# Kernel tuning notes

Measured on AMD Instinct MI355X. Metric: run time of the kernel, lower is better.

The kernel has to match this reference:

```python
import jax, jax.numpy as jnp
import numpy as np

B, E, N, F, D = 4, 8192, 1024, 512, 512
ALPHA = 0.2
NEG = -1e9  # keras Softmax large-negative masking constant


def setup_inputs() -> dict:
    key = jax.random.key(0)
    k_nodes, k_src, k_dst, k_w, k_a = jax.random.split(key, 5)
    nodes = jax.random.normal(k_nodes, (B, N, F), dtype=jnp.float32)
    src = jax.random.randint(k_src, (B, E), 0, N)
    dst = jax.random.randint(k_dst, (B, E), 0, N)
    Cmat = jax.nn.one_hot(src, N, dtype=jnp.float32)  # [B,E,N] source incidence
    Nmat = jax.nn.one_hot(dst, N, dtype=jnp.float32)  # [B,E,N] target incidence
    mask = jnp.ones((B, N, N), dtype=bool)  # present in input tuple but unused by call()
    w = jax.random.normal(k_w, (F, D), dtype=jnp.float32) * 0.05
    attention = jax.random.normal(k_a, (2 * D, 1), dtype=jnp.float32) * 0.05
    return {"nodes": nodes, "Cmat": Cmat, "Nmat": Nmat, "mask": mask,
            "w": w, "attention": attention}


def reference(nodes, Cmat, Nmat, mask, w, attention):
    z = jnp.matmul(nodes, w)                       # [B,N,D]
    z1 = jnp.matmul(Cmat, z)                       # [B,E,D] source embeddings
    z2 = jnp.matmul(Nmat, z)                       # [B,E,D] target embeddings
    couple = jnp.concatenate([z1, z2], axis=-1)    # [B,E,2D]
    att = jax.nn.leaky_relu(jnp.matmul(couple, attention), ALPHA)  # [B,E,1]
    att_t = jnp.swapaxes(att, -1, -2)              # [B,1,E]
    Cmat_t = jnp.swapaxes(Cmat, -1, -2)            # [B,N,E]
    scores = jnp.matmul(Cmat_t * att_t, Nmat)      # [B,N,N] per-edge score scattered
    adj = jnp.matmul(Cmat_t, Nmat)                 # [B,N,N] adjacency
    # keras Softmax(mask=adj): logits += (1 - cast(adj)) * NEG, softmax over last axis
    logits = scores + (1.0 - adj) * (-NEG) * -1.0 if False else scores + (1.0 - adj) * NEG
    adj_norm = jax.nn.softmax(logits, axis=-1) * adj
    out = jax.nn.leaky_relu(jnp.matmul(adj_norm, z), ALPHA)  # [B,N,D]
    return out
```

## Files before the change

### kernel.cpp

```cpp
#include <hip/hip_runtime.h>
#include <hip/hip_bf16.h>
#include <math.h>

#define BB 4
#define EE 8192
#define NN 1024
#define FF 512
#define DD 512
#define ALPHA 0.2f
#define SLOTS 64

typedef __attribute__((ext_vector_type(8))) short short8;
typedef __attribute__((ext_vector_type(4))) float f32x4;

static __device__ __forceinline__ float leaky(float x) { return x > 0.f ? x : ALPHA * x; }

static __device__ __forceinline__ float wave_sum(float v) {
#pragma unroll
    for (int m = 32; m >= 1; m >>= 1) v += __shfl_xor(v, m);
    return v;
}
static __device__ __forceinline__ float wave_max(float v) {
#pragma unroll
    for (int m = 32; m >= 1; m >>= 1) v = fmaxf(v, __shfl_xor(v, m));
    return v;
}
static __device__ __forceinline__ float dot4(float4 a, float4 b) {
    return a.x * b.x + a.y * b.y + a.z * b.z + a.w * b.w;
}
static __device__ __forceinline__ short8 cvt8(float4 a, float4 b) {
    __hip_bfloat16 t[8];
    t[0] = __float2bfloat16(a.x); t[1] = __float2bfloat16(a.y);
    t[2] = __float2bfloat16(a.z); t[3] = __float2bfloat16(a.w);
    t[4] = __float2bfloat16(b.x); t[5] = __float2bfloat16(b.y);
    t[6] = __float2bfloat16(b.z); t[7] = __float2bfloat16(b.w);
    return *(short8*)t;
}
static __device__ __forceinline__ float b2f(short s) {
    unsigned u = ((unsigned)(unsigned short)s) << 16;
    float f;
    __builtin_memcpy(&f, &u, 4);
    return f;
}
static __device__ __forceinline__ short f2b(float f) {
    __hip_bfloat16 h = __float2bfloat16(f);
    short s;
    __builtin_memcpy(&s, &h, 2);
    return s;
}
static __device__ __forceinline__ int find2(uint4 a, uint4 b, int lane) {
    unsigned za = a.x | a.y | a.z | a.w, zb = b.x | b.y | b.z | b.w;
    unsigned long long m = __ballot((za | zb) != 0u);
    if (!m) return -1;
    int il = za ? (lane * 4 + (a.x ? 0 : (a.y ? 1 : (a.z ? 2 : 3))))
                : (256 + lane * 4 + (b.x ? 0 : (b.y ? 1 : (b.z ? 2 : 3))));
    return __shfl(il, (int)__ffsll(m) - 1);
}
static __device__ __forceinline__ int find1(uint4 v, int lane) {
    unsigned nz = v.x | v.y | v.z | v.w;
    unsigned long long m = __ballot(nz != 0u);
    if (!m) return -1;
    int il = lane * 4 + (v.x ? 0 : (v.y ? 1 : (v.z ? 2 : 3)));
    return __shfl(il, (int)__ffsll(m) - 1);
}

__global__ __launch_bounds__(256) void k_prep(const float* __restrict__ w,
                                              const float* __restrict__ attn,
                                              __hip_bfloat16* __restrict__ BT,
                                              float* __restrict__ wa1, float* __restrict__ wa2,
                                              int* __restrict__ cur) {
    int bx = blockIdx.x;
    if (bx < 64) {
        __shared__ float tile[64][65];
        int tk = bx >> 3, tn = bx & 7;
        int k0 = tk * 64, n0 = tn * 64;
#pragma unroll
        for (int it = 0; it < 16; ++it) {
            int id = it * 256 + threadIdx.x;
            int r = id >> 6, c = id & 63;
            tile[r][c] = w[(size_t)(k0 + r) * DD + n0 + c];
        }
        __syncthreads();
#pragma unroll
        for (int it = 0; it < 16; ++it) {
            int id = it * 256 + threadIdx.x;
            int r = id >> 6, c = id & 63;
            BT[(size_t)(n0 + r) * FF + k0 + c] = __float2bfloat16(tile[c][r]);
        }
        return;
    }
    if (bx < 192) {
        int f = (bx - 64) * 4 + (threadIdx.x >> 6);
        int lane = threadIdx.x & 63;
        const float4* wr = (const float4*)(w + (size_t)f * DD);
        const float4* a1p = (const float4*)attn;
        const float4* a2p = (const float4*)(attn + DD);
        float4 wv0 = wr[lane], wv1 = wr[64 + lane];
        float s1 = dot4(wv0, a1p[lane]) + dot4(wv1, a1p[64 + lane]);
        float s2 = dot4(wv0, a2p[lane]) + dot4(wv1, a2p[64 + lane]);
        s1 = wave_sum(s1);
        s2 = wave_sum(s2);
        if (lane == 0) {
            wa1[f] = s1;
            wa2[f] = s2;
        }
        return;
    }
    int4* cp = (int4*)cur;
    int4 z4 = {0, 0, 0, 0};
#pragma unroll
    for (int j = 0; j < 4; j++) cp[threadIdx.x * 4 + j] = z4;
}

#define BM 128
#define BN 64
#define BK 32
#define NEX 8192
__global__ __launch_bounds__(256) void k_mega(const float* __restrict__ nodes,
                                              const __hip_bfloat16* __restrict__ BTbf,
                                              const float* __restrict__ wa1,
                                              const float* __restrict__ wa2,
                                              const float* __restrict__ C,
                                              const float* __restrict__ Nm,
                                              short* __restrict__ Z16,
                                              float* __restrict__ p1, float* __restrict__ p2,
                                              int* __restrict__ cur, int* __restrict__ sDst) {
    __shared__ short As[BM][BK + 8];
    __shared__ short Bs[BN][BK + 8];
    int bx = blockIdx.x;
    int t = threadIdx.x;
    int lane = t & 63;
    if (bx < 256) {
        int m0 = (bx & 31) * BM;
        int n0 = (bx >> 5) * BN;
        int wid = t >> 6;
        int wm = wid & 1, wn = wid >> 1;
        f32x4 acc[4][2] = {};
        const short* Bg = (const short*)BTbf;
        for (int k0 = 0; k0 < FF; k0 += BK) {
#pragma unroll
            for (int s = 0; s < 2; s++) {
                int cid = t + s * 256;
                int r = cid >> 2, cc = cid & 3;
                const float4* ap = (const float4*)&nodes[(size_t)(m0 + r) * FF + k0 + cc * 8];
                *(short8*)&As[r][cc * 8] = cvt8(ap[0], ap[1]);
            }
            {
                int r = t >> 2, cc = t & 3;
                *(short8*)&Bs[r][cc * 8] = *(const short8*)&Bg[(size_t)(n0 + r) * FF + k0 + cc * 8];
            }
            __syncthreads();
            short8 af[4];
            short8 bf[2];
#pragma unroll
            for (int m = 0; m < 4; m++)
                af[m] = *(const short8*)&As[wm * 64 + m * 16 + (lane & 15)][(lane >> 4) * 8];
#pragma unroll
            for (int n = 0; n < 2; n++)
                bf[n] = *(const short8*)&Bs[wn * 32 + n * 16 + (lane & 15)][(lane >> 4) * 8];
#pragma unroll
            for (int m = 0; m < 4; m++)
#pragma unroll
                for (int n = 0; n < 2; n++)
                    acc[m][n] = __builtin_amdgcn_mfma_f32_16x16x32_bf16(af[m], bf[n], acc[m][n], 0, 0, 0);
            __syncthreads();
        }
#pragma unroll
        for (int m = 0; m < 4; m++)
#pragma unroll
            for (int n = 0; n < 2; n++)
#pragma unroll
                for (int r = 0; r < 4; r++) {
                    int row = m0 + wm * 64 + m * 16 + (lane >> 4) * 4 + r;
                    int col = n0 + wn * 32 + n * 16 + (lane & 15);
                    Z16[(size_t)row * DD + col] = f2b(acc[m][n][r]);
                }
        return;
    }
    if (bx < 256 + NEX) {
        int widx = (bx - 256) * 4 + (t >> 6);
        const uint4* rc = (const uint4*)(C + (size_t)widx * NN);
        const uint4* rn = (const uint4*)(Nm + (size_t)widx * NN);
        uint4 a0 = rc[lane], a1 = rc[64 + lane];
        uint4 b0 = rn[lane], b1 = rn[64 + lane];
        int s = find2(a0, a1, lane);
        int d = find2(b0, b1, lane);
#pragma unroll 1
        for (int c = 2; c < 4 && (s < 0 || d < 0); ++c) {
            uint4 va, vb;
            bool needS = s < 0, needD = d < 0;
            if (needS) va = rc[c * 64 + lane];
            if (needD) vb = rn[c * 64 + lane];
            if (needS) {
                int r = find1(va, lane);
                if (r >= 0) s = c * 256 + r;
            }
            if (needD) {
                int r = find1(vb, lane);
                if (r >= 0) d = c * 256 + r;
            }
        }
        if (lane == 0) {
            int b = widx >> 13;
            int row = b * NN + s;
            int pos = atomicAdd(&cur[row], 1);
            if (pos < SLOTS) sDst[row * SLOTS + pos] = d;
        }
        return;
    }
    int rid = (bx - 256 - NEX) * 4 + (t >> 6);
    const float4* nr = (const float4*)(nodes + (size_t)rid * FF);
    const float4* w1p = (const float4*)wa1;
    const float4* w2p = (const float4*)wa2;
    float4 v0 = nr[lane], v1 = nr[64 + lane];
    float s1 = dot4(v0, w1p[lane]) + dot4(v1, w1p[64 + lane]);
    float s2 = dot4(v0, w2p[lane]) + dot4(v1, w2p[64 + lane]);
    s1 = wave_sum(s1);
    s2 = wave_sum(s2);
    if (lane == 0) {
        p1[rid] = s1;
        p2[rid] = s2;
    }
}

__global__ __launch_bounds__(256) void k_out(const int* __restrict__ cur,
                                             const int* __restrict__ sDst,
                                             const float* __restrict__ p1,
                                             const float* __restrict__ p2,
                                             const short* __restrict__ Z16,
                                             float* __restrict__ out) {
    int rid = (blockIdx.x * 256 + threadIdx.x) >> 6;
    int lane = threadIdx.x & 63;
    if (rid >= BB * NN) return;
    int K = cur[rid];
    K = K > SLOTS ? SLOTS : K;
    int base = rid * SLOTS;
    int b = rid >> 10;
    float* op = out + (size_t)rid * DD + lane * 8;
    if (K == 0) {
        float4 z4 = {0.f, 0.f, 0.f, 0.f};
        *(float4*)op = z4;
        *(float4*)(op + 4) = z4;
        return;
    }
    float p1row = p1[rid];
    int de = (lane < K) ? sDst[base + lane] : -1;
    float ae = (lane < K) ? leaky(p1row + p2[(b << 10) + de]) : 0.f;
    float S = 0.f;
    int c = 0, firstk = 64;
    for (int k = 0; k < K; k++) {
        int dk = __shfl(de, k);
        float ak = __shfl(ae, k);
        bool mt = (lane < K) && (dk == de);
        if (mt) {
            S += ak;
            c++;
            if (k < firstk) firstk = k;
        }
    }
    float logit = (lane < K) ? (S + (float)(c - 1) * 1e9f) : -INFINITY;
    float M = wave_max(logit);
    float contrib = (lane < K && firstk == lane) ? __expf(logit - M) : 0.f;
    float Dsum = wave_sum(contrib);
    float wgt = (lane < K) ? __expf(logit - M) / Dsum : 0.f;
    const short* Zb = Z16 + ((size_t)(b << 10)) * DD;
    float acc[8] = {0.f, 0.f, 0.f, 0.f, 0.f, 0.f, 0.f, 0.f};
#pragma unroll
    for (int k = 0; k < 32; k++) {
        if (k >= K) break;
        int dj = __shfl(de, k);
        float wk = __shfl(wgt, k);
        short8 zv = *(const short8*)(Zb + (size_t)dj * DD + lane * 8);
#pragma unroll
        for (int j = 0; j < 8; j++) acc[j] += wk * b2f(zv[j]);
    }
    for (int k = 32; k < K; k++) {
        int dj = __shfl(de, k);
        float wk = __shfl(wgt, k);
        short8 zv = *(const short8*)(Zb + (size_t)dj * DD + lane * 8);
#pragma unroll
        for (int j = 0; j < 8; j++) acc[j] += wk * b2f(zv[j]);
    }
    float4 o0, o1;
    o0.x = leaky(acc[0]); o0.y = leaky(acc[1]); o0.z = leaky(acc[2]); o0.w = leaky(acc[3]);
    o1.x = leaky(acc[4]); o1.y = leaky(acc[5]); o1.z = leaky(acc[6]); o1.w = leaky(acc[7]);
    *(float4*)op = o0;
    *(float4*)(op + 4) = o1;
}

extern "C" void kernel_launch(void* const* d_in, const int* in_sizes, int n_in,
                              void* d_out, int out_size, void* d_ws, size_t ws_size,
                              hipStream_t stream) {
    const float* nodes = (const float*)d_in[0];
    const float* Cmat = (const float*)d_in[1];
    const float* Nmat = (const float*)d_in[2];
    const float* w = (const float*)d_in[4];
    const float* attn = (const float*)d_in[5];
    float* out = (float*)d_out;

    char* ws = (char*)d_ws;
    size_t off = 0;
    auto alloc = [&](size_t bytes) -> void* {
        void* p = ws + off;
        off += (bytes + 255) & ~(size_t)255;
        return p;
    };
    short* Z16 = (short*)alloc((size_t)BB * NN * DD * 2);
    __hip_bfloat16* BT = (__hip_bfloat16*)alloc((size_t)FF * DD * 2);
    float* wa1 = (float*)alloc((size_t)FF * 4);
    float* wa2 = (float*)alloc((size_t)FF * 4);
    int* cur = (int*)alloc((size_t)BB * NN * 4);
    int* sDst = (int*)alloc((size_t)BB * NN * SLOTS * 4);
    float* p1 = (float*)alloc((size_t)BB * NN * 4);
    float* p2 = (float*)alloc((size_t)BB * NN * 4);

    k_prep<<<193, 256, 0, stream>>>(w, attn, BT, wa1, wa2, cur);
    k_mega<<<256 + NEX + 1024, 256, 0, stream>>>(nodes, BT, wa1, wa2, Cmat, Nmat,
                                                 Z16, p1, p2, cur, sDst);
    k_out<<<1024, 256, 0, stream>>>(cur, sDst, p1, p2, Z16, out);
}
```

Measured before the change: 51.58 us.

## Compute attention projections from bf16 Z in output kernel instead of precomputed p1/p2

Drops the w·attention precompute and the per-node p1/p2 dot-product blocks from the prep and mega kernels. The output kernel now computes both attention projections directly from the bf16 Z rows it already gathers, using a wave reduction per neighbour. The edge-scan loop is also simplified to a single loop starting at chunk 0. This cuts blocks and launches in the earlier stages but adds per-neighbour Z loads and reductions in k_out, and the projections now use bf16-rounded Z rather than fp32 nodes.

New measurement: 57.67 us. 11.8% more time.

```diff
diff --git a/kernel.cpp b/kernel.cpp
--- a/kernel.cpp
+++ b/kernel.cpp
@@ -9,6 +9,8 @@
 #define DD 512
 #define ALPHA 0.2f
 #define SLOTS 64
+#define NGEMM 256
+#define NEX 8192
 
 typedef __attribute__((ext_vector_type(8))) short short8;
 typedef __attribute__((ext_vector_type(4))) float f32x4;
@@ -24,9 +26,6 @@
 #pragma unroll
     for (int m = 32; m >= 1; m >>= 1) v = fmaxf(v, __shfl_xor(v, m));
     return v;
-}
-static __device__ __forceinline__ float dot4(float4 a, float4 b) {
-    return a.x * b.x + a.y * b.y + a.z * b.z + a.w * b.w;
 }
 static __device__ __forceinline__ short8 cvt8(float4 a, float4 b) {
     __hip_bfloat16 t[8];
@@ -48,13 +47,9 @@
     __builtin_memcpy(&s, &h, 2);
     return s;
 }
-static __device__ __forceinline__ int find2(uint4 a, uint4 b, int lane) {
-    unsigned za = a.x | a.y | a.z | a.w, zb = b.x | b.y | b.z | b.w;
-    unsigned long long m = __ballot((za | zb) != 0u);
-    if (!m) return -1;
-    int il = za ? (lane * 4 + (a.x ? 0 : (a.y ? 1 : (a.z ? 2 : 3))))
-                : (256 + lane * 4 + (b.x ? 0 : (b.y ? 1 : (b.z ? 2 : 3))));
-    return __shfl(il, (int)__ffsll(m) - 1);
+static __device__ __forceinline__ float dot8(short8 z, float4 alo, float4 ahi) {
+    return b2f(z[0]) * alo.x + b2f(z[1]) * alo.y + b2f(z[2]) * alo.z + b2f(z[3]) * alo.w +
+           b2f(z[4]) * ahi.x + b2f(z[5]) * ahi.y + b2f(z[6]) * ahi.z + b2f(z[7]) * ahi.w;
 }
 static __device__ __forceinline__ int find1(uint4 v, int lane) {
     unsigned nz = v.x | v.y | v.z | v.w;
@@ -65,9 +60,7 @@
 }
 
 __global__ __launch_bounds__(256) void k_prep(const float* __restrict__ w,
-                                              const float* __restrict__ attn,
                                               __hip_bfloat16* __restrict__ BT,
-                                              float* __restrict__ wa1, float* __restrict__ wa2,
                                               int* __restrict__ cur) {
     int bx = blockIdx.x;
     if (bx < 64) {
@@ -89,23 +82,6 @@
         }
         return;
     }
-    if (bx < 192) {
-        int f = (bx - 64) * 4 + (threadIdx.x >> 6);
-        int lane = threadIdx.x & 63;
-        const float4* wr = (const float4*)(w + (size_t)f * DD);
-        const float4* a1p = (const float4*)attn;
-        const float4* a2p = (const float4*)(attn + DD);
-        float4 wv0 = wr[lane], wv1 = wr[64 + lane];
-        float s1 = dot4(wv0, a1p[lane]) + dot4(wv1, a1p[64 + lane]);
-        float s2 = dot4(wv0, a2p[lane]) + dot4(wv1, a2p[64 + lane]);
-        s1 = wave_sum(s1);
-        s2 = wave_sum(s2);
-        if (lane == 0) {
-            wa1[f] = s1;
-            wa2[f] = s2;
-        }
-        return;
-    }
     int4* cp = (int4*)cur;
     int4 z4 = {0, 0, 0, 0};
 #pragma unroll
@@ -115,22 +91,18 @@
 #define BM 128
 #define BN 64
 #define BK 32
-#define NEX 8192
 __global__ __launch_bounds__(256) void k_mega(const float* __restrict__ nodes,
                                               const __hip_bfloat16* __restrict__ BTbf,
-                                              const float* __restrict__ wa1,
-                                              const float* __restrict__ wa2,
                                               const float* __restrict__ C,
                                               const float* __restrict__ Nm,
                                               short* __restrict__ Z16,
-                                              float* __restrict__ p1, float* __restrict__ p2,
                                               int* __restrict__ cur, int* __restrict__ sDst) {
     __shared__ short As[BM][BK + 8];
     __shared__ short Bs[BN][BK + 8];
     int bx = blockIdx.x;
     int t = threadIdx.x;
     int lane = t & 63;
-    if (bx < 256) {
+    if (bx < NGEMM) {
         int m0 = (bx & 31) * BM;
         int n0 = (bx >> 5) * BN;
         int wid = t >> 6;
@@ -177,56 +149,36 @@
                 }
         return;
     }
-    if (bx < 256 + NEX) {
-        int widx = (bx - 256) * 4 + (t >> 6);
-        const uint4* rc = (const uint4*)(C + (size_t)widx * NN);
-        const uint4* rn = (const uint4*)(Nm + (size_t)widx * NN);
-        uint4 a0 = rc[lane], a1 = rc[64 + lane];
-        uint4 b0 = rn[lane], b1 = rn[64 + lane];
-        int s = find2(a0, a1, lane);
-        int d = find2(b0, b1, lane);
+    int widx = (bx - NGEMM) * 4 + (t >> 6);
+    const uint4* rc = (const uint4*)(C + (size_t)widx * NN);
+    const uint4* rn = (const uint4*)(Nm + (size_t)widx * NN);
+    int s = -1, d = -1;
 #pragma unroll 1
-        for (int c = 2; c < 4 && (s < 0 || d < 0); ++c) {
-            uint4 va, vb;
-            bool needS = s < 0, needD = d < 0;
-            if (needS) va = rc[c * 64 + lane];
-            if (needD) vb = rn[c * 64 + lane];
-            if (needS) {
-                int r = find1(va, lane);
-                if (r >= 0) s = c * 256 + r;
-            }
-            if (needD) {
-                int r = find1(vb, lane);
-                if (r >= 0) d = c * 256 + r;
-            }
-        }
-        if (lane == 0) {
-            int b = widx >> 13;
-            int row = b * NN + s;
-            int pos = atomicAdd(&cur[row], 1);
-            if (pos < SLOTS) sDst[row * SLOTS + pos] = d;
-        }
-        return;
-    }
-    int rid = (bx - 256 - NEX) * 4 + (t >> 6);
-    const float4* nr = (const float4*)(nodes + (size_t)rid * FF);
-    const float4* w1p = (const float4*)wa1;
-    const float4* w2p = (const float4*)wa2;
-    float4 v0 = nr[lane], v1 = nr[64 + lane];
-    float s1 = dot4(v0, w1p[lane]) + dot4(v1, w1p[64 + lane]);
-    float s2 = dot4(v0, w2p[lane]) + dot4(v1, w2p[64 + lane]);
-    s1 = wave_sum(s1);
-    s2 = wave_sum(s2);
+    for (int c = 0; c < 4 && ((s < 0) | (d < 0)); ++c) {
+        uint4 va, vb;
+        bool ns = s < 0, nd = d < 0;
+        if (ns) va = rc[c * 64 + lane];
+        if (nd) vb = rn[c * 64 + lane];
+        if (ns) {
+            int r = find1(va, lane);
+            if (r >= 0) s = c * 256 + r;
+        }
+        if (nd) {
+            int r = find1(vb, lane);
+            if (r >= 0) d = c * 256 + r;
+        }
+    }
     if (lane == 0) {
-        p1[rid] = s1;
-        p2[rid] = s2;
+        int b = widx >> 13;
+        int row = b * NN + s;
+        int pos = atomicAdd(&cur[row], 1);
+        if (pos < SLOTS) sDst[row * SLOTS + pos] = d;
     }
 }
 
 __global__ __launch_bounds__(256) void k_out(const int* __restrict__ cur,
                                              const int* __restrict__ sDst,
-                                             const float* __restrict__ p1,
-                                             const float* __restrict__ p2,
+                                             const float* __restrict__ attn,
                                              const short* __restrict__ Z16,
                                              float* __restrict__ out) {
     int rid = (blockIdx.x * 256 + threadIdx.x) >> 6;
@@ -243,9 +195,21 @@
         *(float4*)(op + 4) = z4;
         return;
     }
-    float p1row = p1[rid];
+    const float4* at4 = (const float4*)attn;
+    float4 a1lo = at4[lane * 2], a1hi = at4[lane * 2 + 1];
+    float4 a2lo = at4[128 + lane * 2], a2hi = at4[128 + lane * 2 + 1];
+    const short* Zb = Z16 + ((size_t)(b << 10)) * DD;
+    short8 zr = *(const short8*)(Z16 + (size_t)rid * DD + lane * 8);
+    float p1row = wave_sum(dot8(zr, a1lo, a1hi));
     int de = (lane < K) ? sDst[base + lane] : -1;
-    float ae = (lane < K) ? leaky(p1row + p2[(b << 10) + de]) : 0.f;
+    float p2mine = 0.f;
+    for (int k = 0; k < K; k++) {
+        int dk = __shfl(de, k);
+        short8 zv = *(const short8*)(Zb + (size_t)dk * DD + lane * 8);
+        float sum = wave_sum(dot8(zv, a2lo, a2hi));
+        if (lane == k) p2mine = sum;
+    }
+    float ae = (lane < K) ? leaky(p1row + p2mine) : 0.f;
     float S = 0.f;
     int c = 0, firstk = 64;
     for (int k = 0; k < K; k++) {
@@ -263,7 +227,6 @@
     float contrib = (lane < K && firstk == lane) ? __expf(logit - M) : 0.f;
     float Dsum = wave_sum(contrib);
     float wgt = (lane < K) ? __expf(logit - M) / Dsum : 0.f;
-    const short* Zb = Z16 + ((size_t)(b << 10)) * DD;
     float acc[8] = {0.f, 0.f, 0.f, 0.f, 0.f, 0.f, 0.f, 0.f};
 #pragma unroll
     for (int k = 0; k < 32; k++) {
@@ -307,15 +270,10 @@
     };
     short* Z16 = (short*)alloc((size_t)BB * NN * DD * 2);
     __hip_bfloat16* BT = (__hip_bfloat16*)alloc((size_t)FF * DD * 2);
-    float* wa1 = (float*)alloc((size_t)FF * 4);
-    float* wa2 = (float*)alloc((size_t)FF * 4);
     int* cur = (int*)alloc((size_t)BB * NN * 4);
     int* sDst = (int*)alloc((size_t)BB * NN * SLOTS * 4);
-    float* p1 = (float*)alloc((size_t)BB * NN * 4);
-    float* p2 = (float*)alloc((size_t)BB * NN * 4);
-
-    k_prep<<<193, 256, 0, stream>>>(w, attn, BT, wa1, wa2, cur);
-    k_mega<<<256 + NEX + 1024, 256, 0, stream>>>(nodes, BT, wa1, wa2, Cmat, Nmat,
-                                                 Z16, p1, p2, cur, sDst);
-    k_out<<<1024, 256, 0, stream>>>(cur, sDst, p1, p2, Z16, out);
-}
+
+    k_prep<<<65, 256, 0, stream>>>(w, BT, cur);
+    k_mega<<<NGEMM + NEX, 256, 0, stream>>>(nodes, BT, Cmat, Nmat, Z16, cur, sDst);
+    k_out<<<1024, 256, 0, stream>>>(cur, sDst, attn, Z16, out);
+}
```

## Drop prep kernel: load w directly in GEMM and fuse attention projections into epilogue

Applied to the files above, without the earlier changes.

Removes the separate prep kernel that transposed w to bf16 and computed w·attention. The GEMM now reads fp32 w with strided column loads, converting to bf16 on the fly, and computes p1/p2 in its epilogue from the accumulators via shuffle reductions and atomicAdd. cur, p1 and p2 are zeroed with one memset, which relies on them being contiguous in the workspace. The change saves one launch and the extra per-row dot-product blocks, at the cost of uncoalesced, redundant B loads, float atomics (nondeterministic summation order) and p1/p2 now computed from Z in fp32 accumulators rather than from fp32 nodes.

Measured after the change: 52.42 us. About the same (+1.6%).

```diff
diff --git a/kernel.cpp b/kernel.cpp
--- a/kernel.cpp
+++ b/kernel.cpp
@@ -9,6 +9,8 @@
 #define DD 512
 #define ALPHA 0.2f
 #define SLOTS 64
+#define NGEMM 256
+#define NEX 8192
 
 typedef __attribute__((ext_vector_type(8))) short short8;
 typedef __attribute__((ext_vector_type(4))) float f32x4;
@@ -24,9 +26,6 @@
 #pragma unroll
     for (int m = 32; m >= 1; m >>= 1) v = fmaxf(v, __shfl_xor(v, m));
     return v;
-}
-static __device__ __forceinline__ float dot4(float4 a, float4 b) {
-    return a.x * b.x + a.y * b.y + a.z * b.z + a.w * b.w;
 }
 static __device__ __forceinline__ short8 cvt8(float4 a, float4 b) {
     __hip_bfloat16 t[8];
@@ -64,62 +63,12 @@
     return __shfl(il, (int)__ffsll(m) - 1);
 }
 
-__global__ __launch_bounds__(256) void k_prep(const float* __restrict__ w,
-                                              const float* __restrict__ attn,
-                                              __hip_bfloat16* __restrict__ BT,
-                                              float* __restrict__ wa1, float* __restrict__ wa2,
-                                              int* __restrict__ cur) {
-    int bx = blockIdx.x;
-    if (bx < 64) {
-        __shared__ float tile[64][65];
-        int tk = bx >> 3, tn = bx & 7;
-        int k0 = tk * 64, n0 = tn * 64;
-#pragma unroll
-        for (int it = 0; it < 16; ++it) {
-            int id = it * 256 + threadIdx.x;
-            int r = id >> 6, c = id & 63;
-            tile[r][c] = w[(size_t)(k0 + r) * DD + n0 + c];
-        }
-        __syncthreads();
-#pragma unroll
-        for (int it = 0; it < 16; ++it) {
-            int id = it * 256 + threadIdx.x;
-            int r = id >> 6, c = id & 63;
-            BT[(size_t)(n0 + r) * FF + k0 + c] = __float2bfloat16(tile[c][r]);
-        }
-        return;
-    }
-    if (bx < 192) {
-        int f = (bx - 64) * 4 + (threadIdx.x >> 6);
-        int lane = threadIdx.x & 63;
-        const float4* wr = (const float4*)(w + (size_t)f * DD);
-        const float4* a1p = (const float4*)attn;
-        const float4* a2p = (const float4*)(attn + DD);
-        float4 wv0 = wr[lane], wv1 = wr[64 + lane];
-        float s1 = dot4(wv0, a1p[lane]) + dot4(wv1, a1p[64 + lane]);
-        float s2 = dot4(wv0, a2p[lane]) + dot4(wv1, a2p[64 + lane]);
-        s1 = wave_sum(s1);
-        s2 = wave_sum(s2);
-        if (lane == 0) {
-            wa1[f] = s1;
-            wa2[f] = s2;
-        }
-        return;
-    }
-    int4* cp = (int4*)cur;
-    int4 z4 = {0, 0, 0, 0};
-#pragma unroll
-    for (int j = 0; j < 4; j++) cp[threadIdx.x * 4 + j] = z4;
-}
-
 #define BM 128
 #define BN 64
 #define BK 32
-#define NEX 8192
 __global__ __launch_bounds__(256) void k_mega(const float* __restrict__ nodes,
-                                              const __hip_bfloat16* __restrict__ BTbf,
-                                              const float* __restrict__ wa1,
-                                              const float* __restrict__ wa2,
+                                              const float* __restrict__ w,
+                                              const float* __restrict__ attn,
                                               const float* __restrict__ C,
                                               const float* __restrict__ Nm,
                                               short* __restrict__ Z16,
@@ -130,13 +79,13 @@
     int bx = blockIdx.x;
     int t = threadIdx.x;
     int lane = t & 63;
-    if (bx < 256) {
+    if (bx < NGEMM) {
         int m0 = (bx & 31) * BM;
         int n0 = (bx >> 5) * BN;
         int wid = t >> 6;
         int wm = wid & 1, wn = wid >> 1;
+        int bc = t & 63, bkr = t >> 6;
         f32x4 acc[4][2] = {};
-        const short* Bg = (const short*)BTbf;
         for (int k0 = 0; k0 < FF; k0 += BK) {
 #pragma unroll
             for (int s = 0; s < 2; s++) {
@@ -146,8 +95,11 @@
                 *(short8*)&As[r][cc * 8] = cvt8(ap[0], ap[1]);
             }
             {
-                int r = t >> 2, cc = t & 3;
-                *(short8*)&Bs[r][cc * 8] = *(const short8*)&Bg[(size_t)(n0 + r) * FF + k0 + cc * 8];
+                short tmpb[8];
+#pragma unroll
+                for (int i = 0; i < 8; i++)
+                    tmpb[i] = f2b(w[(size_t)(k0 + bkr * 8 + i) * DD + n0 + bc]);
+                *(short8*)&Bs[bc][bkr * 8] = *(short8*)tmpb;
             }
             __syncthreads();
             short8 af[4];
@@ -165,8 +117,15 @@
                     acc[m][n] = __builtin_amdgcn_mfma_f32_16x16x32_bf16(af[m], bf[n], acc[m][n], 0, 0, 0);
             __syncthreads();
         }
-#pragma unroll
-        for (int m = 0; m < 4; m++)
+        float a1c[2], a2c[2];
+#pragma unroll
+        for (int n = 0; n < 2; n++) {
+            int col = n0 + wn * 32 + n * 16 + (lane & 15);
+            a1c[n] = attn[col];
+            a2c[n] = attn[DD + col];
+        }
+#pragma unroll
+        for (int m = 0; m < 4; m++) {
 #pragma unroll
             for (int n = 0; n < 2; n++)
 #pragma unroll
@@ -175,51 +134,51 @@
                     int col = n0 + wn * 32 + n * 16 + (lane & 15);
                     Z16[(size_t)row * DD + col] = f2b(acc[m][n][r]);
                 }
+#pragma unroll
+            for (int r = 0; r < 4; r++) {
+                float v1 = acc[m][0][r] * a1c[0] + acc[m][1][r] * a1c[1];
+                float v2 = acc[m][0][r] * a2c[0] + acc[m][1][r] * a2c[1];
+#pragma unroll
+                for (int mm = 8; mm >= 1; mm >>= 1) {
+                    v1 += __shfl_xor(v1, mm);
+                    v2 += __shfl_xor(v2, mm);
+                }
+                if ((lane & 15) == 0) {
+                    int row = m0 + wm * 64 + m * 16 + (lane >> 4) * 4 + r;
+                    atomicAdd(&p1[row], v1);
+                    atomicAdd(&p2[row], v2);
+                }
+            }
+        }
         return;
     }
-    if (bx < 256 + NEX) {
-        int widx = (bx - 256) * 4 + (t >> 6);
-        const uint4* rc = (const uint4*)(C + (size_t)widx * NN);
-        const uint4* rn = (const uint4*)(Nm + (size_t)widx * NN);
-        uint4 a0 = rc[lane], a1 = rc[64 + lane];
-        uint4 b0 = rn[lane], b1 = rn[64 + lane];
-        int s = find2(a0, a1, lane);
-        int d = find2(b0, b1, lane);
+    int widx = (bx - NGEMM) * 4 + (t >> 6);
+    const uint4* rc = (const uint4*)(C + (size_t)widx * NN);
+    const uint4* rn = (const uint4*)(Nm + (size_t)widx * NN);
+    uint4 a0 = rc[lane], a1 = rc[64 + lane];
+    uint4 b0 = rn[lane], b1 = rn[64 + lane];
+    int s = find2(a0, a1, lane);
+    int d = find2(b0, b1, lane);
 #pragma unroll 1
-        for (int c = 2; c < 4 && (s < 0 || d < 0); ++c) {
-            uint4 va, vb;
-            bool needS = s < 0, needD = d < 0;
-            if (needS) va = rc[c * 64 + lane];
-            if (needD) vb = rn[c * 64 + lane];
-            if (needS) {
-                int r = find1(va, lane);
-                if (r >= 0) s = c * 256 + r;
-            }
-            if (needD) {
-                int r = find1(vb, lane);
-                if (r >= 0) d = c * 256 + r;
-            }
-        }
-        if (lane == 0) {
-            int b = widx >> 13;
-            int row = b * NN + s;
-            int pos = atomicAdd(&cur[row], 1);
-            if (pos < SLOTS) sDst[row * SLOTS + pos] = d;
-        }
-        return;
-    }
-    int rid = (bx - 256 - NEX) * 4 + (t >> 6);
-    const float4* nr = (const float4*)(nodes + (size_t)rid * FF);
-    const float4* w1p = (const float4*)wa1;
-    const float4* w2p = (const float4*)wa2;
-    float4 v0 = nr[lane], v1 = nr[64 + lane];
-    float s1 = dot4(v0, w1p[lane]) + dot4(v1, w1p[64 + lane]);
-    float s2 = dot4(v0, w2p[lane]) + dot4(v1, w2p[64 + lane]);
-    s1 = wave_sum(s1);
-    s2 = wave_sum(s2);
+    for (int c = 2; c < 4 && (s < 0 || d < 0); ++c) {
+        uint4 va, vb;
+        bool needS = s < 0, needD = d < 0;
+        if (needS) va = rc[c * 64 + lane];
+        if (needD) vb = rn[c * 64 + lane];
+        if (needS) {
+            int r = find1(va, lane);
+            if (r >= 0) s = c * 256 + r;
+        }
+        if (needD) {
+            int r = find1(vb, lane);
+            if (r >= 0) d = c * 256 + r;
+        }
+    }
     if (lane == 0) {
-        p1[rid] = s1;
-        p2[rid] = s2;
+        int b = widx >> 13;
+        int row = b * NN + s;
+        int pos = atomicAdd(&cur[row], 1);
+        if (pos < SLOTS) sDst[row * SLOTS + pos] = d;
     }
 }
 
@@ -306,16 +265,13 @@
         return p;
     };
     short* Z16 = (short*)alloc((size_t)BB * NN * DD * 2);
-    __hip_bfloat16* BT = (__hip_bfloat16*)alloc((size_t)FF * DD * 2);
-    float* wa1 = (float*)alloc((size_t)FF * 4);
-    float* wa2 = (float*)alloc((size_t)FF * 4);
     int* cur = (int*)alloc((size_t)BB * NN * 4);
-    int* sDst = (int*)alloc((size_t)BB * NN * SLOTS * 4);
     float* p1 = (float*)alloc((size_t)BB * NN * 4);
     float* p2 = (float*)alloc((size_t)BB * NN * 4);
-
-    k_prep<<<193, 256, 0, stream>>>(w, attn, BT, wa1, wa2, cur);
-    k_mega<<<256 + NEX + 1024, 256, 0, stream>>>(nodes, BT, wa1, wa2, Cmat, Nmat,
-                                                 Z16, p1, p2, cur, sDst);
+    int* sDst = (int*)alloc((size_t)BB * NN * SLOTS * 4);
+
+    hipMemsetAsync(cur, 0, (size_t)3 * BB * NN * 4, stream);
+    k_mega<<<NGEMM + NEX, 256, 0, stream>>>(nodes, w, attn, Cmat, Nmat,
+                                            Z16, p1, p2, cur, sDst);
     k_out<<<1024, 256, 0, stream>>>(cur, sDst, p1, p2, Z16, out);
 }
```
